# Kernel tuning notes

Measured on AMD Instinct MI355X. Metric: run time of the kernel, lower is better.

The kernel has to match this reference:

```python
import jax, jax.numpy as jnp
import numpy as np

N_NODES = 100000


def _gcn_conv(x, W, b, src, dst, n_nodes):
    """PyG GCNConv: linear -> symmetric norm (with self-loops) -> scatter-add -> bias."""
    h = x @ W  # [N, out]
    # add self-loops
    loop = jnp.arange(n_nodes, dtype=src.dtype)
    s = jnp.concatenate([src, loop])
    d = jnp.concatenate([dst, loop])
    # degree of target nodes (edge weight = 1)
    deg = jax.ops.segment_sum(jnp.ones_like(d, dtype=h.dtype), d, num_segments=n_nodes)
    dinv = jnp.where(deg > 0, jax.lax.rsqrt(jnp.maximum(deg, 1e-12)), 0.0)
    norm = dinv[s] * dinv[d]  # [E+N]
    msg = h[s] * norm[:, None]  # gather + scale
    out = jax.ops.segment_sum(msg, d, num_segments=n_nodes)
    return out + b


def setup_inputs() -> dict:
    key = jax.random.key(0)
    k1, k2, k3, k4 = jax.random.split(key, 4)
    F_IN, HID, OUT, E = 128, 16, 12, 3200000
    x = jax.random.normal(k1, (N_NODES, F_IN), dtype=jnp.float32)
    edge_index = jax.random.randint(k2, (2, E), 0, N_NODES, dtype=jnp.int64)
    W1 = jax.random.normal(k3, (F_IN, HID), dtype=jnp.float32) / np.sqrt(F_IN)
    b1 = jnp.zeros((HID,), dtype=jnp.float32)
    W2 = jax.random.normal(k4, (HID, OUT), dtype=jnp.float32) / np.sqrt(HID)
    b2 = jnp.zeros((OUT,), dtype=jnp.float32)
    return {"x": x, "edge_index": edge_index, "W1": W1, "b1": b1, "W2": W2, "b2": b2}


def reference(x, edge_index, W1, b1, W2, b2):
    src, dst = edge_index[0], edge_index[1]
    h = _gcn_conv(x, W1, b1, src, dst, N_NODES)
    h = jax.nn.relu(h)
    # dropout is identity at inference
    h = _gcn_conv(h, W2, b2, src, dst, N_NODES)
    return jax.nn.log_softmax(h, axis=1)
```

## Files before the change

kernel.cpp:

```cpp
#include <hip/hip_runtime.h>
#include <hip/hip_fp16.h>

#define N_FIN 128
#define N_HID 16
#define N_OUT 12
#define NBLK  1024
#define BN    512
#define STCAP 3200
#define SCAP  17152

__global__ __launch_bounds__(256) void k_binsort(const int* __restrict__ src,
                                                 const int* __restrict__ dst,
                                                 unsigned* __restrict__ hist,
                                                 unsigned* __restrict__ lstart,
                                                 unsigned* __restrict__ bucket_tot,
                                                 unsigned* __restrict__ entries,
                                                 int E, int chunk, int NB) {
  __shared__ unsigned lh[256];
  __shared__ unsigned cur[256];
  __shared__ unsigned stage[STCAP];
  __shared__ unsigned srt[STCAP];
  __shared__ unsigned char bid[STCAP];
  int t = threadIdx.x, blk = blockIdx.x;
  lh[t] = 0u;
  __syncthreads();
  int clo = blk * chunk, chi = min(E, clo + chunk), n = chi - clo;
  for (int j = clo + t; j < chi; j += 256) {
    int d = dst[j], s = src[j];
    int b = d >> 9;
    stage[j - clo] = ((unsigned)s << 9) | (unsigned)(d & (BN - 1));
    bid[j - clo] = (unsigned char)b;
    atomicAdd(&lh[b], 1u);
  }
  __syncthreads();
  unsigned v = lh[t];
  cur[t] = v;
  __syncthreads();
#pragma unroll
  for (int off = 1; off < 256; off <<= 1) {
    unsigned y = (t >= off) ? cur[t - off] : 0u;
    __syncthreads();
    cur[t] += y;
    __syncthreads();
  }
  unsigned excl = cur[t] - v;
  if (t < NB) {
    hist[(size_t)t * NBLK + blk]   = v;
    lstart[(size_t)t * NBLK + blk] = excl;
    if (v) atomicAdd(&bucket_tot[t], v);
  }
  cur[t] = excl;
  __syncthreads();
  for (int i = t; i < n; i += 256) {
    unsigned p = atomicAdd(&cur[bid[i]], 1u);
    srt[p] = stage[i];
  }
  __syncthreads();
  for (int i = t; i < n; i += 256) entries[clo + i] = srt[i];
}

__device__ __forceinline__ int frag_search(const unsigned* cum, unsigned i) {
  int lo = 0, hi = 1024;
  while (hi - lo > 1) { int mid = (lo + hi) >> 1; if (cum[mid] <= i) lo = mid; else hi = mid; }
  return lo;
}

__global__ __launch_bounds__(1024) void k_build(const unsigned* __restrict__ entries,
                                                const unsigned* __restrict__ hist,
                                                const unsigned* __restrict__ lstart,
                                                const unsigned* __restrict__ bucket_tot,
                                                uint2* __restrict__ rsd,
                                                float* __restrict__ dinv,
                                                unsigned* __restrict__ esrc,
                                                int N, int NB, int E, int chunk) {
  __shared__ unsigned cum[1025];
  __shared__ unsigned lst[1024];
  __shared__ unsigned cnt[BN];
  __shared__ unsigned cur[BN];
  __shared__ unsigned raw[SCAP];
  __shared__ unsigned srt[SCAP];
  int t = threadIdx.x, b = blockIdx.x;
  if (t < 256) cur[t] = (t < NB) ? bucket_tot[t] : 0u;
  __syncthreads();
#pragma unroll
  for (int off = 1; off < 256; off <<= 1) {
    unsigned y = 0;
    if (t < 256 && t >= off) y = cur[t - off];
    __syncthreads();
    if (t < 256) cur[t] += y;
    __syncthreads();
  }
  unsigned bstart = (b == 0) ? 0u : cur[b - 1];
  __syncthreads();
  unsigned hv = hist[(size_t)b * NBLK + t];
  lst[t] = lstart[(size_t)b * NBLK + t];
  cum[t] = hv;
  __syncthreads();
#pragma unroll
  for (int off = 1; off < 1024; off <<= 1) {
    unsigned y = (t >= off) ? cum[t - off] : 0u;
    __syncthreads();
    cum[t] += y;
    __syncthreads();
  }
  unsigned incl = cum[t];
  __syncthreads();
  cum[t] = incl - hv;
  if (t == 1023) cum[1024] = incl;
  if (t < BN) cnt[t] = 0u;
  __syncthreads();
  unsigned tot = cum[1024];
  bool fits = (tot <= SCAP);
  for (unsigned i = t; i < tot; i += 1024) {
    int f = frag_search(cum, i);
    unsigned en = entries[(size_t)f * chunk + lst[f] + (i - cum[f])];
    if (fits) raw[i] = en;
    atomicAdd(&cnt[en & (BN - 1)], 1u);
  }
  __syncthreads();
  unsigned v = (t < BN) ? cnt[t] : 0u;
  if (t < BN) cur[t] = v;
  __syncthreads();
#pragma unroll
  for (int off = 1; off < BN; off <<= 1) {
    unsigned y = (t < BN && t >= off) ? cur[t - off] : 0u;
    __syncthreads();
    if (t < BN) cur[t] += y;
    __syncthreads();
  }
  if (t < BN) {
    unsigned excl = cur[t] - v;
    cur[t] = fits ? excl : (bstart + excl);
    int node = b * BN + t;
    if (node < N) {
      rsd[node] = make_uint2(bstart + excl, v);
      dinv[node] = rsqrtf((float)(v + 1u));
    }
  }
  __syncthreads();
  if (fits) {
    for (unsigned i = t; i < tot; i += 1024) {
      unsigned en = raw[i];
      unsigned p = atomicAdd(&cur[en & (BN - 1)], 1u);
      srt[p] = en >> 9;
    }
    __syncthreads();
    for (unsigned i = t; i < tot; i += 1024) esrc[bstart + i] = srt[i];
  } else {
    for (unsigned i = t; i < tot; i += 1024) {
      int f = frag_search(cum, i);
      unsigned en = entries[(size_t)f * chunk + lst[f] + (i - cum[f])];
      unsigned p = atomicAdd(&cur[en & (BN - 1)], 1u);
      esrc[p] = en >> 9;
    }
  }
}

__global__ __launch_bounds__(256) void k_gemm1(const float* __restrict__ x,
                                               const float* __restrict__ W1,
                                               const float* __restrict__ dinv,
                                               __half* __restrict__ hs, int N) {
  __shared__ float xs[16][132];
  __shared__ float wT[16][132];
  int t = threadIdx.x;
#pragma unroll
  for (int i = 0; i < 8; ++i) {
    int idx = t + i * 256;
    int k = idx >> 4, c = idx & 15;
    wT[c][k] = W1[idx];
  }
  int row0 = blockIdx.x * 16;
#pragma unroll
  for (int i = 0; i < 2; ++i) {
    int idx = t + i * 256;
    int r = idx >> 5, c4 = idx & 31;
    float4 v = make_float4(0.f, 0.f, 0.f, 0.f);
    if (row0 + r < N) v = *(const float4*)(x + (size_t)(row0 + r) * N_FIN + c4 * 4);
    *(float4*)&xs[r][c4 * 4] = v;
  }
  __syncthreads();
  int col = t & 15, r = t >> 4;
  float acc = 0.f;
#pragma unroll
  for (int kc = 0; kc < 32; ++kc) {
    float4 xv = *(const float4*)&xs[r][kc * 4];
    float4 wv = *(const float4*)&wT[col][kc * 4];
    acc += xv.x * wv.x + xv.y * wv.y + xv.z * wv.z + xv.w * wv.w;
  }
  int row = row0 + r;
  if (row < N) hs[(size_t)row * N_HID + col] = __float2half(dinv[row] * acc);
}

__device__ __forceinline__ float4 h4f(uint2 v) {
  __half2 h0 = *(__half2*)&v.x, h1 = *(__half2*)&v.y;
  float2 f0 = __half22float2(h0), f1 = __half22float2(h1);
  return make_float4(f0.x, f0.y, f1.x, f1.y);
}
#define ACC(a, v) { float4 f = h4f(v); a.x += f.x; a.y += f.y; a.z += f.z; a.w += f.w; }

__global__ __launch_bounds__(256) void k_gagg1(const unsigned* __restrict__ esrc,
                                               const uint2* __restrict__ rsd,
                                               const uint2* __restrict__ hs,
                                               const float* __restrict__ dinv,
                                               const float* __restrict__ b1,
                                               const float* __restrict__ W2,
                                               __half* __restrict__ hs2, int N) {
  __shared__ float os[32][2][16];
  __shared__ float ro[32][17];
  __shared__ float w2s[N_HID][N_OUT];
  __shared__ float b1s[N_HID];
  int t = threadIdx.x;
  if (t < N_HID * N_OUT) w2s[t / N_OUT][t % N_OUT] = W2[t];
  if (t < N_HID) b1s[t] = b1[t];
  int nl = t >> 3, sub = (t >> 2) & 1, c4 = t & 3;
  int node = blockIdx.x * 32 + nl;
  if (node < N) {
    uint2 rd = rsd[node];
    unsigned s0 = rd.x, dn = rd.y;
    float4 a0 = make_float4(0.f, 0.f, 0.f, 0.f), a1 = a0, a2 = a0, a3 = a0;
    unsigned j = (unsigned)sub;
    for (; j + 6 < dn; j += 8) {
      unsigned e0 = esrc[s0 + j],     e1 = esrc[s0 + j + 2];
      unsigned e2 = esrc[s0 + j + 4], e3 = esrc[s0 + j + 6];
      uint2 v0 = hs[(size_t)e0 * 4 + c4], v1 = hs[(size_t)e1 * 4 + c4];
      uint2 v2 = hs[(size_t)e2 * 4 + c4], v3 = hs[(size_t)e3 * 4 + c4];
      ACC(a0, v0); ACC(a1, v1); ACC(a2, v2); ACC(a3, v3);
    }
    for (; j < dn; j += 2) { uint2 v = hs[(size_t)esrc[s0 + j] * 4 + c4]; ACC(a0, v); }
    if (sub == 0) { uint2 v = hs[(size_t)node * 4 + c4]; ACC(a0, v); }
    int cb = c4 * 4;
    os[nl][sub][cb + 0] = a0.x + a1.x + a2.x + a3.x;
    os[nl][sub][cb + 1] = a0.y + a1.y + a2.y + a3.y;
    os[nl][sub][cb + 2] = a0.z + a1.z + a2.z + a3.z;
    os[nl][sub][cb + 3] = a0.w + a1.w + a2.w + a3.w;
  }
  __syncthreads();
  for (int idx = t; idx < 32 * 16; idx += 256) {
    int n2 = idx >> 4, cc = idx & 15;
    int node2 = blockIdx.x * 32 + n2;
    if (node2 < N)
      ro[n2][cc] = fmaxf(dinv[node2] * (os[n2][0][cc] + os[n2][1][cc]) + b1s[cc], 0.f);
  }
  __syncthreads();
  for (int idx = t; idx < 32 * 16; idx += 256) {
    int n2 = idx >> 4, cc = idx & 15;
    int node2 = blockIdx.x * 32 + n2;
    if (node2 < N) {
      float s = 0.f;
      if (cc < N_OUT) {
#pragma unroll
        for (int k = 0; k < N_HID; ++k) s += ro[n2][k] * w2s[k][cc];
        s *= dinv[node2];
      }
      hs2[(size_t)node2 * N_HID + cc] = __float2half(s);
    }
  }
}

__global__ __launch_bounds__(256) void k_gagg2(const unsigned* __restrict__ esrc,
                                               const uint2* __restrict__ rsd,
                                               const uint2* __restrict__ hs2,
                                               const float* __restrict__ dinv,
                                               const float* __restrict__ b2,
                                               float* __restrict__ out, int N) {
  __shared__ float os[32][2][16];
  __shared__ float zs[32][13];
  __shared__ float ls[32];
  __shared__ float b2s[N_OUT];
  int t = threadIdx.x;
  if (t < N_OUT) b2s[t] = b2[t];
  int nl = t >> 3, sub = (t >> 2) & 1, c4 = t & 3;
  int node = blockIdx.x * 32 + nl;
  if (node < N) {
    uint2 rd = rsd[node];
    unsigned s0 = rd.x, dn = rd.y;
    float4 a0 = make_float4(0.f, 0.f, 0.f, 0.f), a1 = a0, a2 = a0, a3 = a0;
    unsigned j = (unsigned)sub;
    for (; j + 6 < dn; j += 8) {
      unsigned e0 = esrc[s0 + j],     e1 = esrc[s0 + j + 2];
      unsigned e2 = esrc[s0 + j + 4], e3 = esrc[s0 + j + 6];
      uint2 v0 = hs2[(size_t)e0 * 4 + c4], v1 = hs2[(size_t)e1 * 4 + c4];
      uint2 v2 = hs2[(size_t)e2 * 4 + c4], v3 = hs2[(size_t)e3 * 4 + c4];
      ACC(a0, v0); ACC(a1, v1); ACC(a2, v2); ACC(a3, v3);
    }
    for (; j < dn; j += 2) { uint2 v = hs2[(size_t)esrc[s0 + j] * 4 + c4]; ACC(a0, v); }
    if (sub == 0) { uint2 v = hs2[(size_t)node * 4 + c4]; ACC(a0, v); }
    int cb = c4 * 4;
    os[nl][sub][cb + 0] = a0.x + a1.x + a2.x + a3.x;
    os[nl][sub][cb + 1] = a0.y + a1.y + a2.y + a3.y;
    os[nl][sub][cb + 2] = a0.z + a1.z + a2.z + a3.z;
    os[nl][sub][cb + 3] = a0.w + a1.w + a2.w + a3.w;
  }
  __syncthreads();
  for (int idx = t; idx < 32 * N_OUT; idx += 256) {
    int n2 = idx / N_OUT, cc = idx % N_OUT;
    int node2 = blockIdx.x * 32 + n2;
    if (node2 < N)
      zs[n2][cc] = dinv[node2] * (os[n2][0][cc] + os[n2][1][cc]) + b2s[cc];
  }
  __syncthreads();
  if (t < 32) {
    int node2 = blockIdx.x * 32 + t;
    if (node2 < N) {
      float m = zs[t][0];
#pragma unroll
      for (int jj = 1; jj < N_OUT; ++jj) m = fmaxf(m, zs[t][jj]);
      float sum = 0.f;
#pragma unroll
      for (int jj = 0; jj < N_OUT; ++jj) sum += __expf(zs[t][jj] - m);
      ls[t] = m + __logf(sum);
    }
  }
  __syncthreads();
  for (int idx = t; idx < 32 * N_OUT; idx += 256) {
    int n2 = idx / N_OUT, cc = idx % N_OUT;
    int node2 = blockIdx.x * 32 + n2;
    if (node2 < N) out[(size_t)node2 * N_OUT + cc] = zs[n2][cc] - ls[n2];
  }
}

extern "C" void kernel_launch(void* const* d_in, const int* in_sizes, int n_in,
                              void* d_out, int out_size, void* d_ws, size_t ws_size,
                              hipStream_t stream) {
  const float* x  = (const float*)d_in[0];
  const int*   ei = (const int*)d_in[1];
  const float* W1 = (const float*)d_in[2];
  const float* b1 = (const float*)d_in[3];
  const float* W2 = (const float*)d_in[4];
  const float* b2 = (const float*)d_in[5];
  int N = in_sizes[0] / N_FIN;
  int E = in_sizes[1] / 2;
  const int* src = ei;
  const int* dst = ei + E;

  int NB = (N + BN - 1) / BN;
  int M  = NB * NBLK;
  int chunk = (E + NBLK - 1) / NBLK;

  char* ws = (char*)d_ws;
  unsigned* hist       = (unsigned*)ws;  ws += (size_t)M * 4;
  unsigned* lstart     = (unsigned*)ws;  ws += (size_t)M * 4;
  unsigned* bucket_tot = (unsigned*)ws;  ws += 1024;
  float*    dinv       = (float*)ws;     ws += (size_t)N * 4;
  uint2*    rsd        = (uint2*)ws;     ws += (size_t)N * 8;
  size_t big_bytes = (size_t)E * 4;
  size_t hs_bytes  = (size_t)N * N_HID * 2 * 2;
  if (hs_bytes > big_bytes) big_bytes = hs_bytes;
  unsigned* entries = (unsigned*)ws;
  __half*   hs      = (__half*)ws;
  __half*   hs2     = (__half*)(ws + (size_t)N * N_HID * 2);
  ws += big_bytes;
  unsigned* esrc    = (unsigned*)ws;

  hipMemsetAsync(bucket_tot, 0, 1024, stream);
  k_binsort<<<NBLK, 256, 0, stream>>>(src, dst, hist, lstart, bucket_tot, entries, E, chunk, NB);
  k_build  <<<NB, 1024, 0, stream>>>(entries, hist, lstart, bucket_tot, rsd, dinv, esrc,
                                     N, NB, E, chunk);
  k_gemm1  <<<(N + 15) / 16, 256, 0, stream>>>(x, W1, dinv, hs, N);
  k_gagg1  <<<(N + 31) / 32, 256, 0, stream>>>(esrc, rsd, (const uint2*)hs,
                                               dinv, b1, W2, hs2, N);
  k_gagg2  <<<(N + 31) / 32, 256, 0, stream>>>(esrc, rsd, (const uint2*)hs2,
                                               dinv, b2, (float*)d_out, N);
}
```

Measured before the change: 137.6 us.

## Use LUT fragment lookup in build and one-thread-group-per-node aggregation

In k_build, the per-element binary search over fragment prefix sums is replaced by a 1024-entry lookup table plus a short linear correction when the bucket fits in shared memory. The gather kernels now give each node one 4-thread group instead of two interleaved halves, with 8-way unrolled edge loads and 64 nodes per block. The self-loop, normalisation, bias and ReLU are folded into the accumulation epilogue, which removes an extra shared-memory pass and a barrier. The intent is to cut search cost and raise memory-level parallelism per node, at the price of halving the thread count per node and more registers per thread.

After: 139.7 us. No clear change (+1.5%).

```diff
diff --git a/kernel.cpp b/kernel.cpp
--- a/kernel.cpp
+++ b/kernel.cpp
@@ -75,6 +75,7 @@
                                                 int N, int NB, int E, int chunk) {
   __shared__ unsigned cum[1025];
   __shared__ unsigned lst[1024];
+  __shared__ unsigned lut[1024];
   __shared__ unsigned cnt[BN];
   __shared__ unsigned cur[BN];
   __shared__ unsigned raw[SCAP];
@@ -111,11 +112,34 @@
   __syncthreads();
   unsigned tot = cum[1024];
   bool fits = (tot <= SCAP);
-  for (unsigned i = t; i < tot; i += 1024) {
-    int f = frag_search(cum, i);
-    unsigned en = entries[(size_t)f * chunk + lst[f] + (i - cum[f])];
-    if (fits) raw[i] = en;
-    atomicAdd(&cnt[en & (BN - 1)], 1u);
+  if (tot) {
+    unsigned lo = cum[t], hi = cum[t + 1];
+    if (hi > lo) {
+      unsigned k0 = (unsigned)(((unsigned long long)lo * 1024ull + tot - 1) / tot);
+      unsigned k1 = (unsigned)(((unsigned long long)hi * 1024ull + tot - 1) / tot);
+      if (k1 > 1024u) k1 = 1024u;
+      for (unsigned k = k0; k < k1; ++k) lut[k] = (unsigned)t;
+    }
+  }
+  __syncthreads();
+  float scale = tot ? (1024.0f / (float)tot) : 0.f;
+  if (fits) {
+    for (unsigned i = t; i < tot; i += 1024) {
+      unsigned k = (unsigned)((float)i * scale);
+      if (k > 1023u) k = 1023u;
+      int f = (int)lut[k];
+      while (cum[f] > i) --f;
+      while (cum[f + 1] <= i) ++f;
+      unsigned en = entries[(size_t)f * chunk + lst[f] + (i - cum[f])];
+      raw[i] = en;
+      atomicAdd(&cnt[en & (BN - 1)], 1u);
+    }
+  } else {
+    for (unsigned i = t; i < tot; i += 1024) {
+      int f = frag_search(cum, i);
+      unsigned en = entries[(size_t)f * chunk + lst[f] + (i - cum[f])];
+      atomicAdd(&cnt[en & (BN - 1)], 1u);
+    }
   }
   __syncthreads();
   unsigned v = (t < BN) ? cnt[t] : 0u;
@@ -205,51 +229,53 @@
                                                const float* __restrict__ b1,
                                                const float* __restrict__ W2,
                                                __half* __restrict__ hs2, int N) {
-  __shared__ float os[32][2][16];
-  __shared__ float ro[32][17];
+  __shared__ float os[64][17];
   __shared__ float w2s[N_HID][N_OUT];
   __shared__ float b1s[N_HID];
   int t = threadIdx.x;
   if (t < N_HID * N_OUT) w2s[t / N_OUT][t % N_OUT] = W2[t];
   if (t < N_HID) b1s[t] = b1[t];
-  int nl = t >> 3, sub = (t >> 2) & 1, c4 = t & 3;
-  int node = blockIdx.x * 32 + nl;
+  __syncthreads();
+  int nl = t >> 2, c4 = t & 3;
+  int node = blockIdx.x * 64 + nl;
   if (node < N) {
     uint2 rd = rsd[node];
     unsigned s0 = rd.x, dn = rd.y;
     float4 a0 = make_float4(0.f, 0.f, 0.f, 0.f), a1 = a0, a2 = a0, a3 = a0;
-    unsigned j = (unsigned)sub;
-    for (; j + 6 < dn; j += 8) {
-      unsigned e0 = esrc[s0 + j],     e1 = esrc[s0 + j + 2];
-      unsigned e2 = esrc[s0 + j + 4], e3 = esrc[s0 + j + 6];
+    unsigned j = 0;
+    for (; j + 8 <= dn; j += 8) {
+      unsigned e0 = esrc[s0 + j],     e1 = esrc[s0 + j + 1];
+      unsigned e2 = esrc[s0 + j + 2], e3 = esrc[s0 + j + 3];
+      unsigned e4 = esrc[s0 + j + 4], e5 = esrc[s0 + j + 5];
+      unsigned e6 = esrc[s0 + j + 6], e7 = esrc[s0 + j + 7];
       uint2 v0 = hs[(size_t)e0 * 4 + c4], v1 = hs[(size_t)e1 * 4 + c4];
       uint2 v2 = hs[(size_t)e2 * 4 + c4], v3 = hs[(size_t)e3 * 4 + c4];
+      uint2 v4 = hs[(size_t)e4 * 4 + c4], v5 = hs[(size_t)e5 * 4 + c4];
+      uint2 v6 = hs[(size_t)e6 * 4 + c4], v7 = hs[(size_t)e7 * 4 + c4];
       ACC(a0, v0); ACC(a1, v1); ACC(a2, v2); ACC(a3, v3);
-    }
-    for (; j < dn; j += 2) { uint2 v = hs[(size_t)esrc[s0 + j] * 4 + c4]; ACC(a0, v); }
-    if (sub == 0) { uint2 v = hs[(size_t)node * 4 + c4]; ACC(a0, v); }
+      ACC(a0, v4); ACC(a1, v5); ACC(a2, v6); ACC(a3, v7);
+    }
+    for (; j < dn; ++j) {
+      uint2 v = hs[(size_t)esrc[s0 + j] * 4 + c4];
+      ACC(a0, v);
+    }
+    float4 sf = h4f(hs[(size_t)node * 4 + c4]);
+    float di = dinv[node];
     int cb = c4 * 4;
-    os[nl][sub][cb + 0] = a0.x + a1.x + a2.x + a3.x;
-    os[nl][sub][cb + 1] = a0.y + a1.y + a2.y + a3.y;
-    os[nl][sub][cb + 2] = a0.z + a1.z + a2.z + a3.z;
-    os[nl][sub][cb + 3] = a0.w + a1.w + a2.w + a3.w;
-  }
-  __syncthreads();
-  for (int idx = t; idx < 32 * 16; idx += 256) {
+    os[nl][cb + 0] = fmaxf(di * (a0.x + a1.x + a2.x + a3.x + sf.x) + b1s[cb + 0], 0.f);
+    os[nl][cb + 1] = fmaxf(di * (a0.y + a1.y + a2.y + a3.y + sf.y) + b1s[cb + 1], 0.f);
+    os[nl][cb + 2] = fmaxf(di * (a0.z + a1.z + a2.z + a3.z + sf.z) + b1s[cb + 2], 0.f);
+    os[nl][cb + 3] = fmaxf(di * (a0.w + a1.w + a2.w + a3.w + sf.w) + b1s[cb + 3], 0.f);
+  }
+  __syncthreads();
+  for (int idx = t; idx < 64 * 16; idx += 256) {
     int n2 = idx >> 4, cc = idx & 15;
-    int node2 = blockIdx.x * 32 + n2;
-    if (node2 < N)
-      ro[n2][cc] = fmaxf(dinv[node2] * (os[n2][0][cc] + os[n2][1][cc]) + b1s[cc], 0.f);
-  }
-  __syncthreads();
-  for (int idx = t; idx < 32 * 16; idx += 256) {
-    int n2 = idx >> 4, cc = idx & 15;
-    int node2 = blockIdx.x * 32 + n2;
+    int node2 = blockIdx.x * 64 + n2;
     if (node2 < N) {
       float s = 0.f;
       if (cc < N_OUT) {
 #pragma unroll
-        for (int k = 0; k < N_HID; ++k) s += ro[n2][k] * w2s[k][cc];
+        for (int k = 0; k < N_HID; ++k) s += os[n2][k] * w2s[k][cc];
         s *= dinv[node2];
       }
       hs2[(size_t)node2 * N_HID + cc] = __float2half(s);
@@ -263,44 +289,48 @@
                                                const float* __restrict__ dinv,
                                                const float* __restrict__ b2,
                                                float* __restrict__ out, int N) {
-  __shared__ float os[32][2][16];
-  __shared__ float zs[32][13];
-  __shared__ float ls[32];
+  __shared__ float zs[64][13];
+  __shared__ float ls[64];
   __shared__ float b2s[N_OUT];
   int t = threadIdx.x;
   if (t < N_OUT) b2s[t] = b2[t];
-  int nl = t >> 3, sub = (t >> 2) & 1, c4 = t & 3;
-  int node = blockIdx.x * 32 + nl;
+  __syncthreads();
+  int nl = t >> 2, c4 = t & 3;
+  int node = blockIdx.x * 64 + nl;
   if (node < N) {
     uint2 rd = rsd[node];
     unsigned s0 = rd.x, dn = rd.y;
     float4 a0 = make_float4(0.f, 0.f, 0.f, 0.f), a1 = a0, a2 = a0, a3 = a0;
-    unsigned j = (unsigned)sub;
-    for (; j + 6 < dn; j += 8) {
-      unsigned e0 = esrc[s0 + j],     e1 = esrc[s0 + j + 2];
-      unsigned e2 = esrc[s0 + j + 4], e3 = esrc[s0 + j + 6];
+    unsigned j = 0;
+    for (; j + 8 <= dn; j += 8) {
+      unsigned e0 = esrc[s0 + j],     e1 = esrc[s0 + j + 1];
+      unsigned e2 = esrc[s0 + j + 2], e3 = esrc[s0 + j + 3];
+      unsigned e4 = esrc[s0 + j + 4], e5 = esrc[s0 + j + 5];
+      unsigned e6 = esrc[s0 + j + 6], e7 = esrc[s0 + j + 7];
       uint2 v0 = hs2[(size_t)e0 * 4 + c4], v1 = hs2[(size_t)e1 * 4 + c4];
       uint2 v2 = hs2[(size_t)e2 * 4 + c4], v3 = hs2[(size_t)e3 * 4 + c4];
+      uint2 v4 = hs2[(size_t)e4 * 4 + c4], v5 = hs2[(size_t)e5 * 4 + c4];
+      uint2 v6 = hs2[(size_t)e6 * 4 + c4], v7 = hs2[(size_t)e7 * 4 + c4];
       ACC(a0, v0); ACC(a1, v1); ACC(a2, v2); ACC(a3, v3);
-    }
-    for (; j < dn; j += 2) { uint2 v = hs2[(size_t)esrc[s0 + j] * 4 + c4]; ACC(a0, v); }
-    if (sub == 0) { uint2 v = hs2[(size_t)node * 4 + c4]; ACC(a0, v); }
-    int cb = c4 * 4;
-    os[nl][sub][cb + 0] = a0.x + a1.x + a2.x + a3.x;
-    os[nl][sub][cb + 1] = a0.y + a1.y + a2.y + a3.y;
-    os[nl][sub][cb + 2] = a0.z + a1.z + a2.z + a3.z;
-    os[nl][sub][cb + 3] = a0.w + a1.w + a2.w + a3.w;
-  }
-  __syncthreads();
-  for (int idx = t; idx < 32 * N_OUT; idx += 256) {
-    int n2 = idx / N_OUT, cc = idx % N_OUT;
-    int node2 = blockIdx.x * 32 + n2;
-    if (node2 < N)
-      zs[n2][cc] = dinv[node2] * (os[n2][0][cc] + os[n2][1][cc]) + b2s[cc];
-  }
-  __syncthreads();
-  if (t < 32) {
-    int node2 = blockIdx.x * 32 + t;
+      ACC(a0, v4); ACC(a1, v5); ACC(a2, v6); ACC(a3, v7);
+    }
+    for (; j < dn; ++j) {
+      uint2 v = hs2[(size_t)esrc[s0 + j] * 4 + c4];
+      ACC(a0, v);
+    }
+    if (c4 < 3) {
+      float4 sf = h4f(hs2[(size_t)node * 4 + c4]);
+      float di = dinv[node];
+      int cb = c4 * 4;
+      zs[nl][cb + 0] = di * (a0.x + a1.x + a2.x + a3.x + sf.x) + b2s[cb + 0];
+      zs[nl][cb + 1] = di * (a0.y + a1.y + a2.y + a3.y + sf.y) + b2s[cb + 1];
+      zs[nl][cb + 2] = di * (a0.z + a1.z + a2.z + a3.z + sf.z) + b2s[cb + 2];
+      zs[nl][cb + 3] = di * (a0.w + a1.w + a2.w + a3.w + sf.w) + b2s[cb + 3];
+    }
+  }
+  __syncthreads();
+  if (t < 64) {
+    int node2 = blockIdx.x * 64 + t;
     if (node2 < N) {
       float m = zs[t][0];
 #pragma unroll
@@ -312,9 +342,9 @@
     }
   }
   __syncthreads();
-  for (int idx = t; idx < 32 * N_OUT; idx += 256) {
+  for (int idx = t; idx < 64 * N_OUT; idx += 256) {
     int n2 = idx / N_OUT, cc = idx % N_OUT;
-    int node2 = blockIdx.x * 32 + n2;
+    int node2 = blockIdx.x * 64 + n2;
     if (node2 < N) out[(size_t)node2 * N_OUT + cc] = zs[n2][cc] - ls[n2];
   }
 }
@@ -357,8 +387,8 @@
   k_build  <<<NB, 1024, 0, stream>>>(entries, hist, lstart, bucket_tot, rsd, dinv, esrc,
                                      N, NB, E, chunk);
   k_gemm1  <<<(N + 15) / 16, 256, 0, stream>>>(x, W1, dinv, hs, N);
-  k_gagg1  <<<(N + 31) / 32, 256, 0, stream>>>(esrc, rsd, (const uint2*)hs,
+  k_gagg1  <<<(N + 63) / 64, 256, 0, stream>>>(esrc, rsd, (const uint2*)hs,
                                                dinv, b1, W2, hs2, N);
-  k_gagg2  <<<(N + 31) / 32, 256, 0, stream>>>(esrc, rsd, (const uint2*)hs2,
+  k_gagg2  <<<(N + 63) / 64, 256, 0, stream>>>(esrc, rsd, (const uint2*)hs2,
                                                dinv, b2, (float*)d_out, N);
 }
```
